# Performance work log

Hardware: AMD Instinct MI355X
Metric: run time of the kernel (lower is better)

The kernel has to match this reference:

```python
import jax, jax.numpy as jnp
import numpy as np

HEADS = 8
DIM_HEAD = 64
GAMMA = 0.01
LAMBDA_REG = 0.001
EPS = 1e-6


def layer_norm(x, g, b, eps=1e-5):
    mu = x.mean(-1, keepdims=True)
    var = jnp.var(x, axis=-1, keepdims=True)
    return (x - mu) * jax.lax.rsqrt(var + eps) * g + b


def setup_inputs() -> dict:
    key = jax.random.key(0)
    ks = jax.random.split(key, 20)
    B, N, DIM = 8, 1024, 512
    d = DIM_HEAD
    inner = HEADS * d
    inp = {}
    inp["q"] = jax.random.normal(ks[0], (B, N, DIM), jnp.float32)
    inp["k"] = jax.random.normal(ks[1], (B, N, DIM), jnp.float32)
    inp["v"] = jax.random.normal(ks[2], (B, N, DIM), jnp.float32)
    # input_linear: LayerNorm(dim) + Linear(dim -> inner, no bias)
    inp["ln_g"] = jnp.ones((DIM,), jnp.float32)
    inp["ln_b"] = jnp.zeros((DIM,), jnp.float32)
    inp["W_in"] = jax.random.normal(ks[3], (DIM, inner), jnp.float32) * 0.02
    # weight_predictor: Linear(2d->d), LN(d), ReLU, Linear(d->d//2), ReLU, Linear(d//2->3), Softmax
    inp["wp_W1"] = jax.random.normal(ks[4], (2 * d, d), jnp.float32) * 0.05
    inp["wp_b1"] = jnp.zeros((d,), jnp.float32)
    inp["wp_ln_g"] = jnp.ones((d,), jnp.float32)
    inp["wp_ln_b"] = jnp.zeros((d,), jnp.float32)
    inp["wp_W2"] = jax.random.normal(ks[5], (d, d // 2), jnp.float32) * 0.05
    inp["wp_b2"] = jnp.zeros((d // 2,), jnp.float32)
    inp["wp_W3"] = jax.random.normal(ks[6], (d // 2, 3), jnp.float32) * 0.05
    inp["wp_b3"] = jnp.zeros((3,), jnp.float32)
    inp["weight_temp"] = jnp.ones((1,), jnp.float32) * 2.0
    # output_linear: Linear(inner -> dim) with bias
    inp["W_out"] = jax.random.normal(ks[7], (inner, DIM), jnp.float32) * 0.02
    inp["b_out"] = jnp.zeros((DIM,), jnp.float32)
    return inp


def reference(q, k, v, ln_g, ln_b, W_in, wp_W1, wp_b1, wp_ln_g, wp_ln_b,
              wp_W2, wp_b2, wp_W3, wp_b3, weight_temp, W_out, b_out):
    H, d = HEADS, DIM_HEAD
    B, N, _ = q.shape

    def proj(t):
        x = layer_norm(t, ln_g, ln_b) @ W_in          # [B, N, H*d]
        return x.reshape(B, N, H, d).transpose(2, 0, 1, 3)  # h q n d

    f_q, f_k, f_v = proj(q), proj(k), proj(v)
    m = f_k.shape[2]

    # --- cosine component (cosine_distance with clamp to [-0.95, 0.95]) ---
    dots_raw = jnp.einsum('hbnd,hbmd->hbnm', f_q, f_k)
    n1 = jnp.linalg.norm(f_q, axis=-1, keepdims=True) + EPS      # h b n 1
    n2 = jnp.linalg.norm(f_k, axis=-1) + EPS                      # h b m
    cosine_sim = jnp.clip(dots_raw / (n1 * n2[:, :, None, :]), -0.95, 0.95)

    # --- regularized covariance component ---
    f_k_c = f_k - f_k.mean(axis=2, keepdims=True)
    f_q_c = f_q - f_q.mean(axis=-1, keepdims=True)
    cov = jnp.einsum('hbnd,hbmd->hbnm', f_q_c, f_k_c) / (d ** 0.5 + 1e-6)
    cov = jnp.clip((LAMBDA_REG / max(m, 1)) * cov, -20.0, 20.0)

    # --- margin-based variance component (eval: adaptive_gamma == gamma) ---
    fqn = f_q / jnp.maximum(jnp.linalg.norm(f_q, axis=-1, keepdims=True), EPS)
    fkn = f_k / jnp.maximum(jnp.linalg.norm(f_k, axis=-1, keepdims=True), EPS)
    cs = jnp.clip(jnp.einsum('hbnd,hbmd->hbnm', fqn, fkn), -0.95, 0.95)
    margin = jnp.clip(GAMMA - cs, 0.0, 5.0)
    var_full = jnp.broadcast_to(margin.mean(axis=-1, keepdims=True), cs.shape)

    # --- dynamic weight mixing ---
    q_g = f_q.mean(axis=(1, 2))   # [h, d]
    k_g = f_k.mean(axis=(1, 2))
    z = jnp.concatenate([q_g, k_g], axis=-1) @ wp_W1 + wp_b1
    z = jax.nn.relu(layer_norm(z, wp_ln_g, wp_ln_b))
    z = jax.nn.relu(z @ wp_W2 + wp_b2)
    p = jax.nn.softmax(z @ wp_W3 + wp_b3, axis=-1)   # predictor ends with Softmax
    wt = jnp.clip(weight_temp, 0.1, 10.0)
    w = jax.nn.softmax(p / wt, axis=-1)               # second softmax, as in torch
    w = w * (1.0 - 3 * 0.1) + 0.1                     # [h, 3]
    cw = w[:, 0][:, None, None, None]
    covw = w[:, 1][:, None, None, None]
    vw = w[:, 2][:, None, None, None]

    sg = jax.lax.stop_gradient
    std1 = lambda x: jnp.std(x, ddof=1)               # torch.std is unbiased
    cos_n = sg(std1(cosine_sim)) + EPS
    cov_n = sg(std1(cov)) + EPS
    var_n = sg(std1(var_full)) + EPS

    dots = cw * (cosine_sim / cos_n) + covw * (cov / cov_n * 0.3) + vw * (var_full / var_n * 0.3)
    temp = jnp.clip(0.5 + sg(std1(dots)), 0.3, 3.0)
    dots = dots / temp

    out = jnp.einsum('hbnm,hbmd->hbnd', jax.nn.softmax(dots, axis=-1), f_v)
    out = out.transpose(1, 2, 0, 3).reshape(B, N, H * d)
    return out @ W_out + b_out
```

## Files before the change

kernel.cpp:

```cpp
#include <hip/hip_runtime.h>
#include <math.h>

#define H_ 8
#define B_ 8
#define N_ 1024
#define D_ 64
#define DIMM 512
#define NROWS 8192

typedef __attribute__((ext_vector_type(8))) short s8v;
typedef __attribute__((ext_vector_type(4))) float f4v;
typedef __attribute__((ext_vector_type(2))) unsigned int u2v;
union fragu { s8v v; unsigned int w[4]; uint4 q; };

#define BMFMA(a, b, c) __builtin_amdgcn_mfma_f32_16x16x32_bf16(a, b, c, 0, 0, 0)

__device__ __forceinline__ float wred_sum(float v) {
#pragma unroll
    for (int m = 32; m >= 1; m >>= 1) v += __shfl_xor(v, m, 64);
    return v;
}
__device__ __forceinline__ double wred_sum_d(double v) {
#pragma unroll
    for (int m = 32; m >= 1; m >>= 1) v += __shfl_xor(v, m, 64);
    return v;
}
__device__ __forceinline__ unsigned cvtpk(float a, float b) {
    unsigned r;
    asm("v_cvt_pk_bf16_f32 %0, %1, %2" : "=v"(r) : "v"(a), "v"(b));
    return r;
}
__device__ __forceinline__ void bsplit(float a, unsigned short& hi, unsigned short& lo) {
    unsigned h = cvtpk(a, 0.f);
    hi = (unsigned short)h;
    float r = a - __uint_as_float(h << 16);
    lo = (unsigned short)cvtpk(r, 0.f);
}
__device__ __forceinline__ void split8(const float* a, unsigned* hw, unsigned* lw) {
#pragma unroll
    for (int i = 0; i < 4; ++i) {
        unsigned h = cvtpk(a[2 * i], a[2 * i + 1]);
        hw[i] = h;
        float l0 = a[2 * i]     - __uint_as_float(h << 16);
        float l1 = a[2 * i + 1] - __uint_as_float(h & 0xFFFF0000u);
        lw[i] = cvtpk(l0, l1);
    }
}

__device__ __forceinline__ float fexp2(float x) {
#if __has_builtin(__builtin_amdgcn_exp2f)
    return __builtin_amdgcn_exp2f(x);
#else
    return exp2f(x);
#endif
}

#if __has_builtin(__builtin_amdgcn_permlane16_swap) && __has_builtin(__builtin_amdgcn_permlane32_swap)
#define HAVE_PLSWAP 1
#endif

__device__ __forceinline__ float kbmax4(float x) {
#ifdef HAVE_PLSWAP
    u2v a = __builtin_amdgcn_permlane16_swap(__float_as_uint(x), __float_as_uint(x), false, false);
    float m = fmaxf(__uint_as_float(a[0]), __uint_as_float(a[1]));
    u2v c = __builtin_amdgcn_permlane32_swap(__float_as_uint(m), __float_as_uint(m), false, false);
    return fmaxf(__uint_as_float(c[0]), __uint_as_float(c[1]));
#else
    x = fmaxf(x, __shfl_xor(x, 16, 64));
    return fmaxf(x, __shfl_xor(x, 32, 64));
#endif
}
__device__ __forceinline__ float kbsum4(float x) {
#ifdef HAVE_PLSWAP
    u2v a = __builtin_amdgcn_permlane16_swap(__float_as_uint(x), __float_as_uint(x), false, false);
    float m = __uint_as_float(a[0]) + __uint_as_float(a[1]);
    u2v c = __builtin_amdgcn_permlane32_swap(__float_as_uint(m), __float_as_uint(m), false, false);
    return __uint_as_float(c[0]) + __uint_as_float(c[1]);
#else
    x += __shfl_xor(x, 16, 64);
    x += __shfl_xor(x, 32, 64);
    return x;
#endif
}

__global__ __launch_bounds__(256) void k_prep(
    const float* __restrict__ q, const float* __restrict__ k, const float* __restrict__ v,
    float* __restrict__ muv, float* __restrict__ rsd,
    const float* __restrict__ Win, const float* __restrict__ Wout,
    unsigned short* __restrict__ Wthi, unsigned short* __restrict__ Wtlo,
    unsigned short* __restrict__ Wothi, unsigned short* __restrict__ Wotlo)
{
    int bx = blockIdx.x;
    __shared__ float S[64][65];
    int t = threadIdx.x;
    if (bx < 6144) {
        int w = t >> 6, lane = t & 63;
        int row = bx * 4 + w;
        int tens = row >> 13;
        int lrow = row & 8191;
        const float* src = (tens == 0) ? q : (tens == 1 ? k : v);
        const float* p = src + (long long)lrow * DIMM + lane * 8;
        float4 a = *(const float4*)p;
        float4 b = *(const float4*)(p + 4);
        float s  = a.x + a.y + a.z + a.w + b.x + b.y + b.z + b.w;
        float sq = a.x*a.x + a.y*a.y + a.z*a.z + a.w*a.w + b.x*b.x + b.y*b.y + b.z*b.z + b.w*b.w;
        s = wred_sum(s); sq = wred_sum(sq);
        if (lane == 0) {
            float m = s * (1.f / 512.f);
            float var = sq * (1.f / 512.f) - m * m;
            muv[row] = m;
            rsd[row] = rsqrtf(var + 1e-5f);
        }
        return;
    }
    int sb = bx - 6144;
    int z = sb >> 6;
    int rem = sb & 63;
    int kxi = rem & 7, jxi = rem >> 3;
    const float* Wsrc = z ? Wout : Win;
    unsigned short* Dhi = z ? Wothi : Wthi;
    unsigned short* Dlo = z ? Wotlo : Wtlo;
    int k0 = kxi * 64, j0 = jxi * 64;
    int rr = t >> 2, seg = t & 3;
    const float* p = Wsrc + (long long)(k0 + rr) * DIMM + j0 + seg * 16;
    float4 a0 = *(const float4*)p, a1 = *(const float4*)(p + 4),
           a2 = *(const float4*)(p + 8), a3 = *(const float4*)(p + 12);
    S[rr][seg*16+ 0]=a0.x; S[rr][seg*16+ 1]=a0.y; S[rr][seg*16+ 2]=a0.z; S[rr][seg*16+ 3]=a0.w;
    S[rr][seg*16+ 4]=a1.x; S[rr][seg*16+ 5]=a1.y; S[rr][seg*16+ 6]=a1.z; S[rr][seg*16+ 7]=a1.w;
    S[rr][seg*16+ 8]=a2.x; S[rr][seg*16+ 9]=a2.y; S[rr][seg*16+10]=a2.z; S[rr][seg*16+11]=a2.w;
    S[rr][seg*16+12]=a3.x; S[rr][seg*16+13]=a3.y; S[rr][seg*16+14]=a3.z; S[rr][seg*16+15]=a3.w;
    __syncthreads();
    float f[16];
#pragma unroll
    for (int i = 0; i < 16; ++i) f[i] = S[seg * 16 + i][rr];
    unsigned hw[8], lw[8];
    split8(f, hw, lw);
    split8(f + 8, hw + 4, lw + 4);
    long long ob = (long long)(j0 + rr) * DIMM + k0 + seg * 16;
    *(uint4*)&Dhi[ob]     = make_uint4(hw[0], hw[1], hw[2], hw[3]);
    *(uint4*)&Dhi[ob + 8] = make_uint4(hw[4], hw[5], hw[6], hw[7]);
    *(uint4*)&Dlo[ob]     = make_uint4(lw[0], lw[1], lw[2], lw[3]);
    *(uint4*)&Dlo[ob + 8] = make_uint4(lw[4], lw[5], lw[6], lw[7]);
}

__global__ __launch_bounds__(256) void k_gemm_in(
    const float* __restrict__ qx, const float* __restrict__ kx, const float* __restrict__ vx,
    const float* __restrict__ muv, const float* __restrict__ rsd,
    const float* __restrict__ lng, const float* __restrict__ lnb,
    const unsigned short* __restrict__ Wthi, const unsigned short* __restrict__ Wtlo,
    unsigned short* __restrict__ Fqhi, unsigned short* __restrict__ Fqlo,
    unsigned short* __restrict__ Fkhi, unsigned short* __restrict__ Fklo,
    unsigned short* __restrict__ Fvthi, unsigned short* __restrict__ Fvtlo,
    float* __restrict__ qinv, float* __restrict__ mq,
    float* __restrict__ kinv, float* __restrict__ ks,
    float* __restrict__ csq, float* __restrict__ csk)
{
    int tens = blockIdx.z;
    const float* X = (tens == 0) ? qx : (tens == 1 ? kx : vx);
    int row0 = blockIdx.x * 128, hq = blockIdx.y;
    const float* muT = muv + tens * NROWS;
    const float* rsT = rsd + tens * NROWS;
    __shared__ unsigned short Ah[128][32], Al[128][32];
    __shared__ unsigned short Bh[128][32], Bl[128][32];
    int t = threadIdx.x;
    int w = t >> 6, lane = t & 63, l15 = lane & 15, kb = lane >> 4;
    int srow = t >> 1, sseg = t & 1;
    int sw = (srow >> 1) & 3;
    int c0 = ((2 * sseg + 0) ^ sw) * 8;
    int c1 = ((2 * sseg + 1) ^ sw) * 8;
    int rs = (l15 >> 1) & 3;
    int rb = (kb ^ rs) * 8;
    float amu = muT[row0 + srow], ars = rsT[row0 + srow];
    f4v acc[2][8];
#pragma unroll
    for (int rt = 0; rt < 2; ++rt)
#pragma unroll
        for (int dt = 0; dt < 8; ++dt) acc[rt][dt] = (f4v){0.f, 0.f, 0.f, 0.f};

    float4 x0, x1, x2, x3, g0, g1, g2, g3, cc0, cc1, cc2, cc3;
    uint4 wh0, wh1, wl0, wl1;
#define GIN_LOAD(KC) { \
    int kO = (KC) * 32 + sseg * 16; \
    const float* xp = X + (long long)(row0 + srow) * DIMM + kO; \
    x0 = *(const float4*)xp;       x1 = *(const float4*)(xp + 4); \
    x2 = *(const float4*)(xp + 8); x3 = *(const float4*)(xp + 12); \
    g0 = *(const float4*)(lng + kO);     g1 = *(const float4*)(lng + kO + 4); \
    g2 = *(const float4*)(lng + kO + 8); g3 = *(const float4*)(lng + kO + 12); \
    cc0 = *(const float4*)(lnb + kO);     cc1 = *(const float4*)(lnb + kO + 4); \
    cc2 = *(const float4*)(lnb + kO + 8); cc3 = *(const float4*)(lnb + kO + 12); \
    const unsigned short* wph = Wthi + (long long)(hq * 128 + srow) * DIMM + kO; \
    const unsigned short* wpl = Wtlo + (long long)(hq * 128 + srow) * DIMM + kO; \
    wh0 = *(const uint4*)wph; wh1 = *(const uint4*)(wph + 8); \
    wl0 = *(const uint4*)wpl; wl1 = *(const uint4*)(wpl + 8); }

    GIN_LOAD(0)
    for (int kc = 0; kc < 16; ++kc) {
        float av[16];
        av[ 0]=fmaf((x0.x-amu)*ars,g0.x,cc0.x); av[ 1]=fmaf((x0.y-amu)*ars,g0.y,cc0.y);
        av[ 2]=fmaf((x0.z-amu)*ars,g0.z,cc0.z); av[ 3]=fmaf((x0.w-amu)*ars,g0.w,cc0.w);
        av[ 4]=fmaf((x1.x-amu)*ars,g1.x,cc1.x); av[ 5]=fmaf((x1.y-amu)*ars,g1.y,cc1.y);
        av[ 6]=fmaf((x1.z-amu)*ars,g1.z,cc1.z); av[ 7]=fmaf((x1.w-amu)*ars,g1.w,cc1.w);
        av[ 8]=fmaf((x2.x-amu)*ars,g2.x,cc2.x); av[ 9]=fmaf((x2.y-amu)*ars,g2.y,cc2.y);
        av[10]=fmaf((x2.z-amu)*ars,g2.z,cc2.z); av[11]=fmaf((x2.w-amu)*ars,g2.w,cc2.w);
        av[12]=fmaf((x3.x-amu)*ars,g3.x,cc3.x); av[13]=fmaf((x3.y-amu)*ars,g3.y,cc3.y);
        av[14]=fmaf((x3.z-amu)*ars,g3.z,cc3.z); av[15]=fmaf((x3.w-amu)*ars,g3.w,cc3.w);
        unsigned hw[8], lw[8];
        split8(av, hw, lw);
        split8(av + 8, hw + 4, lw + 4);
        *(uint4*)&Ah[srow][c0] = make_uint4(hw[0], hw[1], hw[2], hw[3]);
        *(uint4*)&Ah[srow][c1] = make_uint4(hw[4], hw[5], hw[6], hw[7]);
        *(uint4*)&Al[srow][c0] = make_uint4(lw[0], lw[1], lw[2], lw[3]);
        *(uint4*)&Al[srow][c1] = make_uint4(lw[4], lw[5], lw[6], lw[7]);
        *(uint4*)&Bh[srow][c0] = wh0;
        *(uint4*)&Bh[srow][c1] = wh1;
        *(uint4*)&Bl[srow][c0] = wl0;
        *(uint4*)&Bl[srow][c1] = wl1;
        __syncthreads();
        if (kc < 15) { GIN_LOAD(kc + 1) }
        fragu ah[2], al2[2];
#pragma unroll
        for (int rt = 0; rt < 2; ++rt) {
            ah[rt].v  = *(const s8v*)&Ah[w * 32 + rt * 16 + l15][rb];
            al2[rt].v = *(const s8v*)&Al[w * 32 + rt * 16 + l15][rb];
        }
#pragma unroll
        for (int dt = 0; dt < 8; ++dt) {
            s8v bh = *(const s8v*)&Bh[dt * 16 + l15][rb];
            s8v bl = *(const s8v*)&Bl[dt * 16 + l15][rb];
#pragma unroll
            for (int rt = 0; rt < 2; ++rt) {
                acc[rt][dt] = BMFMA(ah[rt].v, bh, acc[rt][dt]);
                acc[rt][dt] = BMFMA(ah[rt].v, bl, acc[rt][dt]);
                acc[rt][dt] = BMFMA(al2[rt].v, bh, acc[rt][dt]);
            }
        }
        __syncthreads();
    }
#undef GIN_LOAD
    int b = row0 >> 10;
    if (tens < 2) {
        unsigned short* Dh = tens ? Fkhi : Fqhi;
        unsigned short* Dl = tens ? Fklo : Fqlo;
#pragma unroll
        for (int rt = 0; rt < 2; ++rt) {
            int nloc = (row0 & 1023) + w * 32 + rt * 16 + kb * 4;
#pragma unroll
            for (int dt = 0; dt < 8; ++dt) {
                int hb = (hq * 2 + (dt >> 2)) * 8 + b;
#pragma unroll
                for (int r = 0; r < 4; ++r) {
                    unsigned short hi, lo;
                    bsplit(acc[rt][dt][r], hi, lo);
                    long long idx = ((long long)hb * N_ + nloc + r) * D_ + (dt & 3) * 16 + l15;
                    Dh[idx] = hi;
                    Dl[idx] = lo;
                }
            }
#pragma unroll
            for (int hh = 0; hh < 2; ++hh) {
                int hb2 = (hq * 2 + hh) * 8 + b;
#pragma unroll
                for (int r = 0; r < 4; ++r) {
                    float a0 = acc[rt][hh*4+0][r], a1 = acc[rt][hh*4+1][r],
                          a2 = acc[rt][hh*4+2][r], a3 = acc[rt][hh*4+3][r];
                    float s  = a0 + a1 + a2 + a3;
                    float sq = a0*a0 + a1*a1 + a2*a2 + a3*a3;
#pragma unroll
                    for (int msk = 8; msk >= 1; msk >>= 1) {
                        s  += __shfl_xor(s, msk, 64);
                        sq += __shfl_xor(sq, msk, 64);
                    }
                    if (l15 == 0) {
                        int rowg = hb2 * N_ + nloc + r;
                        float inv = 1.f / (sqrtf(sq) + 1e-6f);
                        if (tens) { kinv[rowg] = inv; ks[rowg] = s; }
                        else      { qinv[rowg] = inv; mq[rowg] = s * (1.f / 64.f); }
                    }
                }
            }
        }
        float* cs = tens ? csk : csq;
#pragma unroll
        for (int dt = 0; dt < 8; ++dt) {
            int hb2 = (hq * 2 + (dt >> 2)) * 8 + b;
            float c = acc[0][dt][0] + acc[0][dt][1] + acc[0][dt][2] + acc[0][dt][3]
                    + acc[1][dt][0] + acc[1][dt][1] + acc[1][dt][2] + acc[1][dt][3];
            c += __shfl_xor(c, 16, 64);
            c += __shfl_xor(c, 32, 64);
            if (kb == 0) atomicAdd(&cs[hb2 * 64 + (dt & 3) * 16 + l15], c);
        }
    } else {
#pragma unroll
        for (int dt = 0; dt < 8; ++dt) {
            int hb = (hq * 2 + (dt >> 2)) * 8 + b;
#pragma unroll
            for (int rt = 0; rt < 2; ++rt) {
                int vcol = (row0 & 1023) + (w >> 1) * 64 + (w & 1) * 32 + (kb << 3) + (rt << 2);
                unsigned short hh4[4], ll4[4];
#pragma unroll
                for (int r = 0; r < 4; ++r) bsplit(acc[rt][dt][r], hh4[r], ll4[r]);
                long long idx = ((long long)hb * D_ + (dt & 3) * 16 + l15) * N_ + vcol;
                *(uint2*)&Fvthi[idx] = make_uint2((unsigned)hh4[0] | ((unsigned)hh4[1] << 16),
                                                  (unsigned)hh4[2] | ((unsigned)hh4[3] << 16));
                *(uint2*)&Fvtlo[idx] = make_uint2((unsigned)ll4[0] | ((unsigned)ll4[1] << 16),
                                                  (unsigned)ll4[2] | ((unsigned)ll4[3] << 16));
            }
        }
    }
}

__global__ __launch_bounds__(512) void k_gvec_mlp(
    const unsigned short* __restrict__ Fqhi, const unsigned short* __restrict__ Fqlo,
    const float* __restrict__ csk, const float* __restrict__ mq, float* __restrict__ g,
    const float* __restrict__ csq,
    const float* __restrict__ W1, const float* __restrict__ b1,
    const float* __restrict__ lg, const float* __restrict__ lb,
    const float* __restrict__ W2, const float* __restrict__ b2,
    const float* __restrict__ W3, const float* __restrict__ b3,
    const float* __restrict__ wtemp, float* __restrict__ wbuf)
{
    int bx = blockIdx.x;
    int t = threadIdx.x;
    if (bx < 128) {
        __shared__ float mk[64];
        __shared__ float smkv;
        int hb = bx >> 1;
        int r0 = (bx & 1) * 512;
        if (t < 64) mk[t] = csk[hb * 64 + t] * (1.f / 1024.f);
        __syncthreads();
        if (t == 0) {
            float s = 0;
            for (int i = 0; i < 64; ++i) s += mk[i];
            smkv = s;
        }
        __syncthreads();
        float smk = smkv;
        int rowg = hb * N_ + r0 + t;
        const uint4* ph = (const uint4*)(Fqhi + (long long)rowg * D_);
        const uint4* pl = (const uint4*)(Fqlo + (long long)rowg * D_);
        float acc = 0.f;
#pragma unroll
        for (int i = 0; i < 8; ++i) {
            uint4 hh = ph[i];
            uint4 ll = pl[i];
            const unsigned* hu = &hh.x;
            const unsigned* lu = &ll.x;
#pragma unroll
            for (int j = 0; j < 4; ++j) {
                float v0 = __uint_as_float((hu[j] & 0xFFFFu) << 16) + __uint_as_float((lu[j] & 0xFFFFu) << 16);
                float v1 = __uint_as_float(hu[j] & 0xFFFF0000u) + __uint_as_float(lu[j] & 0xFFFF0000u);
                acc = fmaf(v0, mk[i * 8 + j * 2], acc);
                acc = fmaf(v1, mk[i * 8 + j * 2 + 1], acc);
            }
        }
        g[rowg] = acc - mq[rowg] * smk;
        return;
    }
    __shared__ float cat[8][128];
    __shared__ float z1[8][64];
    __shared__ float zr[8][64];
    __shared__ float z2[8][32];
    __shared__ float z3[8][3];
    __shared__ float lnmu[8], lnrs[8];
    {
        int h = t >> 6, dd = t & 63;
        float sq = 0, sk = 0;
        for (int b = 0; b < 8; ++b) {
            sq += csq[(h * 8 + b) * 64 + dd];
            sk += csk[(h * 8 + b) * 64 + dd];
        }
        cat[h][dd]      = sq * (1.f / 8192.f);
        cat[h][64 + dd] = sk * (1.f / 8192.f);
    }
    __syncthreads();
    {
        int h = t >> 6, j = t & 63;
        float a = b1[j];
        for (int i = 0; i < 128; ++i) a = fmaf(cat[h][i], W1[i * 64 + j], a);
        z1[h][j] = a;
    }
    __syncthreads();
    if (t < 8) {
        float m = 0;
        for (int j = 0; j < 64; ++j) m += z1[t][j];
        m *= (1.f / 64.f);
        float v2 = 0;
        for (int j = 0; j < 64; ++j) { float d = z1[t][j] - m; v2 += d * d; }
        v2 *= (1.f / 64.f);
        lnmu[t] = m; lnrs[t] = rsqrtf(v2 + 1e-5f);
    }
    __syncthreads();
    {
        int h = t >> 6, j = t & 63;
        float z = (z1[h][j] - lnmu[h]) * lnrs[h] * lg[j] + lb[j];
        zr[h][j] = fmaxf(z, 0.f);
    }
    __syncthreads();
    if (t < 256) {
        int h = t >> 5, j2 = t & 31;
        float a = b2[j2];
        for (int j = 0; j < 64; ++j) a = fmaf(zr[h][j], W2[j * 32 + j2], a);
        z2[h][j2] = fmaxf(a, 0.f);
    }
    __syncthreads();
    if (t < 24) {
        int h = t / 3, c = t % 3;
        float a = b3[c];
        for (int j2 = 0; j2 < 32; ++j2) a = fmaf(z2[h][j2], W3[j2 * 3 + c], a);
        z3[h][c] = a;
    }
    __syncthreads();
    if (t < 8) {
        int h = t;
        float wt = fminf(fmaxf(wtemp[0], 0.1f), 10.f);
        float a = z3[h][0], b = z3[h][1], c = z3[h][2];
        float mx = fmaxf(a, fmaxf(b, c));
        float ea = expf(a - mx), eb = expf(b - mx), ec = expf(c - mx);
        float s = ea + eb + ec;
        float p0 = ea / s, p1 = eb / s, p2 = ec / s;
        float q0 = p0 / wt, q1 = p1 / wt, q2 = p2 / wt;
        mx = fmaxf(q0, fmaxf(q1, q2));
        ea = expf(q0 - mx); eb = expf(q1 - mx); ec = expf(q2 - mx);
        s = ea + eb + ec;
        wbuf[h * 3 + 0] = (ea / s) * 0.7f + 0.1f;
        wbuf[h * 3 + 1] = (eb / s) * 0.7f + 0.1f;
        wbuf[h * 3 + 2] = (ec / s) * 0.7f + 0.1f;
    }
}

__global__ __launch_bounds__(256) void k_pass1(
    const unsigned short* __restrict__ Fqhi, const unsigned short* __restrict__ Fkhi,
    const float* __restrict__ qinvA, const float* __restrict__ mqA, const float* __restrict__ gA,
    const float* __restrict__ kinvA, const float* __restrict__ ksA,
    float* __restrict__ rowA, float* __restrict__ rowM,
    double* __restrict__ accum)
{
    int bx = blockIdx.x;
    int loc = bx >> 3;
    int hb = (bx & 7) * 8 + (loc >> 6);
    int rem = loc & 63;
    int n0 = (rem >> 2) * 64;
    int mtc = rem & 3;
    int h = hb >> 3;
    __shared__ unsigned short Khi[64][72];
    __shared__ float ki1s[64], ksls[64];
    __shared__ double wsum[4][4];
    int t = threadIdx.x;
    int w = t >> 6, lane = t & 63, l15 = lane & 15, kb = lane >> 4;
    int srow = t >> 2, seg = t & 3;
    const float SC = (float)((0.001 / 1024.0) / (8.0 + 1e-6));

    fragu qh[2];
    {
        long long qbase = ((long long)hb * N_ + n0 + w * 16 + l15) * D_;
#pragma unroll
        for (int k2 = 0; k2 < 2; ++k2)
            qh[k2].q = *(const uint4*)(Fqhi + qbase + k2 * 32 + kb * 8);
    }
    float qi1_r[4], qm_r[4], qgs_r[4];
#pragma unroll
    for (int r = 0; r < 4; ++r) {
        int rowg = hb * N_ + n0 + w * 16 + kb * 4 + r;
        qi1_r[r] = qinvA[rowg];
        qm_r[r]  = mqA[rowg];
        qgs_r[r] = gA[rowg] * SC;
    }
    float sacc[5][4] = {};

    for (int mt = mtc * 4; mt < mtc * 4 + 4; ++mt) {
        {
            long long kro = ((long long)hb * N_ + mt * 64 + srow) * D_ + seg * 16;
            uint4 h0 = *(const uint4*)(Fkhi + kro), h1 = *(const uint4*)(Fkhi + kro + 8);
            *(uint4*)&Khi[srow][seg * 16]     = h0;
            *(uint4*)&Khi[srow][seg * 16 + 8] = h1;
            if (t < 64) {
                ki1s[t] = kinvA[hb * N_ + mt * 64 + t];
                ksls[t] = ksA[hb * N_ + mt * 64 + t];
            }
        }
        __syncthreads();
#pragma unroll
        for (int nt = 0; nt < 4; ++nt) {
            f4v acc = {0.f, 0.f, 0.f, 0.f};
            s8v kh0 = *(const s8v*)&Khi[nt * 16 + l15][kb * 8];
            s8v kh1 = *(const s8v*)&Khi[nt * 16 + l15][32 + kb * 8];
            acc = BMFMA(qh[0].v, kh0, acc);
            acc = BMFMA(qh[1].v, kh1, acc);
            int key = nt * 16 + l15;
            float k1 = ki1s[key];
            float ksvSC = ksls[key] * SC;
            float e_r[4];
#pragma unroll
            for (int r = 0; r < 4; ++r) e_r[r] = fmaf(qm_r[r], ksvSC, qgs_r[r]);
#pragma unroll
            for (int r = 0; r < 4; ++r) {
                float dv = acc[r];
                float A  = dv * qi1_r[r] * k1;
                float Bv = fmaf(dv, SC, -e_r[r]);
                sacc[0][r] += A;
                sacc[1][r] = fmaf(A, A, sacc[1][r]);
                sacc[2][r] = fmaf(Bv, Bv, sacc[2][r]);
                sacc[3][r] = fmaf(A, Bv, sacc[3][r]);
                sacc[4][r] += fminf(A, 0.01f);
            }
        }
        __syncthreads();
    }
    {
        const int map[4] = {0, 3, 4, 6};
#pragma unroll
        for (int qq = 0; qq < 4; ++qq) {
            float s = sacc[qq][0] + sacc[qq][1] + sacc[qq][2] + sacc[qq][3];
            double d = wred_sum_d((double)s);
            if (lane == 0) wsum[qq][w] = d;
        }
        __syncthreads();
        if (t < 4) {
            double tot = wsum[t][0] + wsum[t][1] + wsum[t][2] + wsum[t][3];
            atomicAdd(&accum[h * 9 + map[t]], tot);
        }
    }
    float vA[4], vM[4];
#pragma unroll
    for (int r = 0; r < 4; ++r) {
        float a = sacc[0][r], m = sacc[4][r];
#pragma unroll
        for (int msk = 8; msk >= 1; msk >>= 1) {
            a += __shfl_xor(a, msk, 64);
            m += __shfl_xor(m, msk, 64);
        }
        vA[r] = a; vM[r] = m;
    }
    if (l15 == 0) {
#pragma unroll
        for (int r = 0; r < 4; ++r) {
            int rowg = hb * N_ + n0 + w * 16 + kb * 4 + r;
            atomicAdd(&rowA[rowg], vA[r]);
            atomicAdd(&rowM[rowg], 2.56f - vM[r]);
        }
    }
}

__global__ __launch_bounds__(256) void k_rowfin(
    const float* __restrict__ rowA, const float* __restrict__ rowM,
    float* __restrict__ varC, double* __restrict__ accum,
    const float* __restrict__ wbuf, float* __restrict__ scl,
    unsigned* __restrict__ ticket)
{
    int hb = blockIdx.x;
    int h = hb >> 3;
    int t = threadIdx.x;
    int w = t >> 6, lane = t & 63;
    __shared__ double wsum[3][4];
    double c2 = 0, c5 = 0, c7 = 0;
    for (int i = t; i < N_; i += 256) {
        int idx = hb * N_ + i;
        float rm = rowM[idx];
        float C = rm * (1.f / 1024.f);
        varC[idx] = C;
        c2 += (double)rm;
        c5 += (double)rm * (double)C;
        c7 += (double)C * (double)rowA[idx];
    }
    c2 = wred_sum_d(c2); c5 = wred_sum_d(c5); c7 = wred_sum_d(c7);
    if (lane == 0) { wsum[0][w] = c2; wsum[1][w] = c5; wsum[2][w] = c7; }
    __syncthreads();
    if (t < 3) {
        const int map[3] = {2, 5, 7};
        double tot = wsum[t][0] + wsum[t][1] + wsum[t][2] + wsum[t][3];
        atomicAdd(&accum[h * 9 + map[t]], tot);
    }
    __syncthreads();
    __shared__ unsigned lastv;
    if (t == 0) {
        __threadfence();
        lastv = atomicAdd(ticket, 1u);
    }
    __syncthreads();
    if (lastv != 63 || t != 0) return;

    double av[8][9];
#pragma unroll
    for (int hh = 0; hh < 8; ++hh)
#pragma unroll
        for (int j = 0; j < 9; ++j)
            av[hh][j] = __hip_atomic_load(&accum[hh * 9 + j], __ATOMIC_RELAXED, __HIP_MEMORY_SCOPE_AGENT);
    const double T = 67108864.0;
    double GA = 0, GB = 0, GC = 0, GAA = 0, GBB = 0, GCC = 0;
#pragma unroll
    for (int hh = 0; hh < 8; ++hh) {
        GA += av[hh][0]; GB += av[hh][1]; GC += av[hh][2];
        GAA += av[hh][3]; GBB += av[hh][4]; GCC += av[hh][5];
    }
    double cos_n = sqrt(fmax((GAA - GA * GA / T) / (T - 1.0), 0.0)) + 1e-6;
    double cov_n = sqrt(fmax((GBB - GB * GB / T) / (T - 1.0), 0.0)) + 1e-6;
    double var_n = sqrt(fmax((GCC - GC * GC / T) / (T - 1.0), 0.0)) + 1e-6;
    double sd = 0, sd2 = 0;
    double al[8], be[8], ga[8];
#pragma unroll
    for (int hh = 0; hh < 8; ++hh) {
        al[hh] = (double)wbuf[hh * 3 + 0] / cos_n;
        be[hh] = (double)wbuf[hh * 3 + 1] * 0.3 / cov_n;
        ga[hh] = (double)wbuf[hh * 3 + 2] * 0.3 / var_n;
        sd  += al[hh] * av[hh][0] + be[hh] * av[hh][1] + ga[hh] * av[hh][2];
        sd2 += al[hh] * al[hh] * av[hh][3] + be[hh] * be[hh] * av[hh][4] + ga[hh] * ga[hh] * av[hh][5]
             + 2.0 * al[hh] * be[hh] * av[hh][6] + 2.0 * al[hh] * ga[hh] * av[hh][7]
             + 2.0 * be[hh] * ga[hh] * av[hh][8];
    }
    double vard = fmax((sd2 - sd * sd / T) / (T - 1.0), 0.0);
    double temp = 0.5 + sqrt(vard);
    temp = fmin(fmax(temp, 0.3), 3.0);
#pragma unroll
    for (int hh = 0; hh < 8; ++hh) {
        scl[hh * 3 + 0] = (float)(al[hh] / temp);
        scl[hh * 3 + 1] = (float)(be[hh] / temp);
        scl[hh * 3 + 2] = (float)(ga[hh] / temp);
    }
}

__global__ __launch_bounds__(512) void k_pass2(
    const unsigned short* __restrict__ Fqhi, const unsigned short* __restrict__ Fqlo,
    const unsigned short* __restrict__ Fkhi, const unsigned short* __restrict__ Fklo,
    const unsigned short* __restrict__ Fvthi, const unsigned short* __restrict__ Fvtlo,
    const float* __restrict__ qinvA, const float* __restrict__ mqA, const float* __restrict__ gA,
    const float* __restrict__ kinvA, const float* __restrict__ ksA,
    const float* __restrict__ varC, const float* __restrict__ scl,
    unsigned short* __restrict__ attn_hi, unsigned short* __restrict__ attn_lo)
{
    int bx = blockIdx.x;
    int g = bx >> 3;
    int hb = (bx & 7) * 8 + (g >> 3);
    int n0 = (g & 7) * 128;
    int h = hb >> 3, b = hb & 7;
    __shared__ unsigned short Khi[2][64][72];
    __shared__ unsigned short Klo[2][64][72];
    __shared__ unsigned short Vh[2][64][72];
    __shared__ unsigned short Vl[2][64][72];
    __shared__ float ki1s[2][64], ksls[2][64];
    int t = threadIdx.x;
    int w = t >> 6, lane = t & 63, l15 = lane & 15, kb = lane >> 4;
    int srow = t >> 3, sc = (t & 7) * 8;
    const float SC = (float)((0.001 / 1024.0) / (8.0 + 1e-6));
    const float L2E = 1.44269504f;
    float sAh = scl[h*3+0] * L2E, sBh = scl[h*3+1] * L2E, sCh = scl[h*3+2] * L2E;

    fragu qh[2], ql[2];
    {
        long long qbase = ((long long)hb * N_ + n0 + w * 16 + l15) * D_;
#pragma unroll
        for (int k2 = 0; k2 < 2; ++k2) {
            qh[k2].q = *(const uint4*)(Fqhi + qbase + k2 * 32 + kb * 8);
            ql[k2].q = *(const uint4*)(Fqlo + qbase + k2 * 32 + kb * 8);
        }
    }
    int rowq = hb * N_ + n0 + w * 16 + l15;
    float qiA  = qinvA[rowq] * sAh;
    float SCb  = SC * sBh;
    float nqmS = -mqA[rowq] * SCb;
    float cb  = fmaf(sCh, varC[rowq], -(gA[rowq] * SC) * sBh);

    float Mr = -1e30f, Lr = 0.f;
    f4v oacc[4];
#pragma unroll
    for (int dt = 0; dt < 4; ++dt) oacc[dt] = (f4v){0.f, 0.f, 0.f, 0.f};
    int idxr[4];
#pragma unroll
    for (int r = 0; r < 4; ++r) idxr[r] = (kb * 20 + r) * 4;

    uint4 rkh, rkl, rvh, rvl;
    float rki, rks;
#define P2_LOAD(MT) { \
    long long kro = ((long long)hb * N_ + (MT) * 64 + srow) * D_ + sc; \
    rkh = *(const uint4*)(Fkhi + kro); rkl = *(const uint4*)(Fklo + kro); \
    long long vro = ((long long)hb * D_ + srow) * N_ + (MT) * 64 + sc; \
    rvh = *(const uint4*)(Fvthi + vro); rvl = *(const uint4*)(Fvtlo + vro); \
    if (t < 64) { rki = kinvA[hb * N_ + (MT) * 64 + t]; rks = ksA[hb * N_ + (MT) * 64 + t]; } }

    P2_LOAD(0)
    for (int mt = 0; mt < 16; ++mt) {
        int buf = mt & 1;
        *(uint4*)&Khi[buf][srow][sc] = rkh;
        *(uint4*)&Klo[buf][srow][sc] = rkl;
        *(uint4*)&Vh[buf][srow][sc]  = rvh;
        *(uint4*)&Vl[buf][srow][sc]  = rvl;
        if (t < 64) { ki1s[buf][t] = rki; ksls[buf][t] = rks; }
        __syncthreads();
        if (mt < 15) { P2_LOAD(mt + 1) }
        float p[4][4];
#pragma unroll
        for (int nt = 0; nt < 4; ++nt) {
            f4v acc = {0.f, 0.f, 0.f, 0.f};
            __builtin_amdgcn_s_setprio(1);
#pragma unroll
            for (int k2 = 0; k2 < 2; ++k2) {
                s8v kh = *(const s8v*)&Khi[buf][nt * 16 + l15][k2 * 32 + kb * 8];
                s8v kl = *(const s8v*)&Klo[buf][nt * 16 + l15][k2 * 32 + kb * 8];
                acc = BMFMA(kh, qh[k2].v, acc);
                acc = BMFMA(kh, ql[k2].v, acc);
                acc = BMFMA(kl, qh[k2].v, acc);
            }
            __builtin_amdgcn_s_setprio(0);
            float4 k1v = *(const float4*)&ki1s[buf][nt * 16 + kb * 4];
            float4 ksv = *(const float4*)&ksls[buf][nt * 16 + kb * 4];
            float k1a[4] = {k1v.x, k1v.y, k1v.z, k1v.w};
            float ksa[4] = {ksv.x, ksv.y, ksv.z, ksv.w};
#pragma unroll
            for (int r = 0; r < 4; ++r) {
                float qks = fmaf(qiA, k1a[r], SCb);
                float cbk = fmaf(nqmS, ksa[r], cb);
                p[nt][r] = fmaf(acc[r], qks, cbk);
            }
        }
        float tmax = fmaxf(fmaxf(fmaxf(p[0][0], p[0][1]), fmaxf(p[0][2], p[0][3])),
                           fmaxf(fmaxf(p[1][0], p[1][1]), fmaxf(p[1][2], p[1][3])));
        tmax = fmaxf(tmax, fmaxf(fmaxf(fmaxf(p[2][0], p[2][1]), fmaxf(p[2][2], p[2][3])),
                                 fmaxf(fmaxf(p[3][0], p[3][1]), fmaxf(p[3][2], p[3][3]))));
        tmax = kbmax4(tmax);
        if (__any(tmax - Mr > 11.5415605f)) {
            float nM = fmaxf(Mr, tmax);
            float scf = fexp2(Mr - nM);
            Mr = nM;
            Lr *= scf;
            float scr[4];
#pragma unroll
            for (int r = 0; r < 4; ++r)
                scr[r] = __int_as_float(__builtin_amdgcn_ds_bpermute(idxr[r], __float_as_int(scf)));
#pragma unroll
            for (int dt = 0; dt < 4; ++dt)
#pragma unroll
                for (int r = 0; r < 4; ++r) oacc[dt][r] *= scr[r];
        }
        float ps = 0.f;
#pragma unroll
        for (int nt = 0; nt < 4; ++nt)
#pragma unroll
            for (int r = 0; r < 4; ++r) {
                float e = fexp2(p[nt][r] - Mr);
                p[nt][r] = e;
                ps += e;
            }
        ps = kbsum4(ps);
        Lr += ps;
        fragu pah[2], pal[2];
#pragma unroll
        for (int k2 = 0; k2 < 2; ++k2) {
#pragma unroll
            for (int j = 0; j < 4; ++j) {
                float x = p[2 * k2 + (j >> 1)][(j & 1) * 2];
                float y = p[2 * k2 + (j >> 1)][(j & 1) * 2 + 1];
                unsigned hw2 = cvtpk(x, y);
                pah[k2].w[j] = hw2;
                float lx = x - __uint_as_float(hw2 << 16);
                float ly = y - __uint_as_float(hw2 & 0xFFFF0000u);
                pal[k2].w[j] = cvtpk(lx, ly);
            }
        }
        __builtin_amdgcn_s_setprio(1);
#pragma unroll
        for (int dt = 0; dt < 4; ++dt) {
#pragma unroll
            for (int k2 = 0; k2 < 2; ++k2) {
                s8v vh2 = *(const s8v*)&Vh[buf][dt * 16 + l15][k2 * 32 + kb * 8];
                s8v vl2 = *(const s8v*)&Vl[buf][dt * 16 + l15][k2 * 32 + kb * 8];
                oacc[dt] = BMFMA(pah[k2].v, vh2, oacc[dt]);
                oacc[dt] = BMFMA(pah[k2].v, vl2, oacc[dt]);
                oacc[dt] = BMFMA(pal[k2].v, vh2, oacc[dt]);
            }
        }
        __builtin_amdgcn_s_setprio(0);
    }
#undef P2_LOAD
    float inv_r[4];
#pragma unroll
    for (int r = 0; r < 4; ++r) {
        float Lq = __int_as_float(__builtin_amdgcn_ds_bpermute(idxr[r], __float_as_int(Lr)));
        inv_r[r] = 1.f / Lq;
    }
#pragma unroll
    for (int dt = 0; dt < 4; ++dt)
#pragma unroll
        for (int r = 0; r < 4; ++r) {
            float o = oacc[dt][r] * inv_r[r];
            unsigned short hi, lo;
            bsplit(o, hi, lo);
            long long idx = ((long long)(b * N_ + n0 + w * 16 + kb * 4 + r)) * DIMM + h * 64 + dt * 16 + l15;
            attn_hi[idx] = hi;
            attn_lo[idx] = lo;
        }
}

__global__ __launch_bounds__(256) void k_gemm_out(
    const unsigned short* __restrict__ Ahi, const unsigned short* __restrict__ Alo,
    const unsigned short* __restrict__ Wothi, const unsigned short* __restrict__ Wotlo,
    const float* __restrict__ bias, float* __restrict__ out)
{
    int row0 = blockIdx.x * 128, j0 = blockIdx.y * 128;
    __shared__ unsigned short Ah[128][32], Al[128][32];
    __shared__ unsigned short Bh[128][32], Bl[128][32];
    int t = threadIdx.x;
    int w = t >> 6, lane = t & 63, l15 = lane & 15, kb = lane >> 4;
    int srow = t >> 1, sseg = t & 1;
    int sw = (srow >> 1) & 3;
    int c0 = ((2 * sseg + 0) ^ sw) * 8;
    int c1 = ((2 * sseg + 1) ^ sw) * 8;
    int rs = (l15 >> 1) & 3;
    int rb = (kb ^ rs) * 8;
    f4v acc[2][8];
#pragma unroll
    for (int rt = 0; rt < 2; ++rt)
#pragma unroll
        for (int dt = 0; dt < 8; ++dt) acc[rt][dt] = (f4v){0.f, 0.f, 0.f, 0.f};
    uint4 a0, a1, al0, al1, b0, b1, bl0, bl1;
#define GOUT_LOAD(KC) { \
    int kO = (KC) * 32 + sseg * 16; \
    const unsigned short* ap  = Ahi + (long long)(row0 + srow) * DIMM + kO; \
    const unsigned short* alp = Alo + (long long)(row0 + srow) * DIMM + kO; \
    a0 = *(const uint4*)ap;  a1 = *(const uint4*)(ap + 8); \
    al0 = *(const uint4*)alp; al1 = *(const uint4*)(alp + 8); \
    const unsigned short* bp  = Wothi + (long long)(j0 + srow) * DIMM + kO; \
    const unsigned short* blp = Wotlo + (long long)(j0 + srow) * DIMM + kO; \
    b0 = *(const uint4*)bp;  b1 = *(const uint4*)(bp + 8); \
    bl0 = *(const uint4*)blp; bl1 = *(const uint4*)(blp + 8); }

    GOUT_LOAD(0)
    for (int kc = 0; kc < 16; ++kc) {
        *(uint4*)&Ah[srow][c0] = a0;
        *(uint4*)&Ah[srow][c1] = a1;
        *(uint4*)&Al[srow][c0] = al0;
        *(uint4*)&Al[srow][c1] = al1;
        *(uint4*)&Bh[srow][c0] = b0;
        *(uint4*)&Bh[srow][c1] = b1;
        *(uint4*)&Bl[srow][c0] = bl0;
        *(uint4*)&Bl[srow][c1] = bl1;
        __syncthreads();
        if (kc < 15) { GOUT_LOAD(kc + 1) }
        fragu ah[2], al2[2];
#pragma unroll
        for (int rt = 0; rt < 2; ++rt) {
            ah[rt].v  = *(const s8v*)&Ah[w * 32 + rt * 16 + l15][rb];
            al2[rt].v = *(const s8v*)&Al[w * 32 + rt * 16 + l15][rb];
        }
#pragma unroll
        for (int dt = 0; dt < 8; ++dt) {
            s8v bh = *(const s8v*)&Bh[dt * 16 + l15][rb];
            s8v bl = *(const s8v*)&Bl[dt * 16 + l15][rb];
#pragma unroll
            for (int rt = 0; rt < 2; ++rt) {
                acc[rt][dt] = BMFMA(ah[rt].v, bh, acc[rt][dt]);
                acc[rt][dt] = BMFMA(ah[rt].v, bl, acc[rt][dt]);
                acc[rt][dt] = BMFMA(al2[rt].v, bh, acc[rt][dt]);
            }
        }
        __syncthreads();
    }
#undef GOUT_LOAD
#pragma unroll
    for (int dt = 0; dt < 8; ++dt) {
        float bv = bias[j0 + dt * 16 + l15];
#pragma unroll
        for (int rt = 0; rt < 2; ++rt)
#pragma unroll
            for (int r = 0; r < 4; ++r)
                out[(long long)(row0 + w * 32 + rt * 16 + kb * 4 + r) * DIMM + j0 + dt * 16 + l15]
                    = acc[rt][dt][r] + bv;
    }
}

extern "C" void kernel_launch(void* const* d_in, const int* in_sizes, int n_in,
                              void* d_out, int out_size, void* d_ws, size_t ws_size,
                              hipStream_t stream) {
    (void)in_sizes; (void)n_in; (void)out_size; (void)ws_size;
    const float* q      = (const float*)d_in[0];
    const float* k      = (const float*)d_in[1];
    const float* v      = (const float*)d_in[2];
    const float* ln_g   = (const float*)d_in[3];
    const float* ln_b   = (const float*)d_in[4];
    const float* W_in   = (const float*)d_in[5];
    const float* wp_W1  = (const float*)d_in[6];
    const float* wp_b1  = (const float*)d_in[7];
    const float* wp_lng = (const float*)d_in[8];
    const float* wp_lnb = (const float*)d_in[9];
    const float* wp_W2  = (const float*)d_in[10];
    const float* wp_b2  = (const float*)d_in[11];
    const float* wp_W3  = (const float*)d_in[12];
    const float* wp_b3  = (const float*)d_in[13];
    const float* wtemp  = (const float*)d_in[14];
    const float* W_out  = (const float*)d_in[15];
    const float* b_out  = (const float*)d_in[16];
    float* out = (float*)d_out;

    char* w = (char*)d_ws;
    unsigned short* attn_hi = (unsigned short*)(w + 0);
    unsigned short* attn_lo = (unsigned short*)(w + 8388608);
    unsigned short* Fqhi  = (unsigned short*)(w + 16777216);
    unsigned short* Fqlo  = (unsigned short*)(w + 25165824);
    unsigned short* Fkhi  = (unsigned short*)(w + 33554432);
    unsigned short* Fklo  = (unsigned short*)(w + 41943040);
    unsigned short* Fvthi = (unsigned short*)(w + 50331648);
    unsigned short* Fvtlo = (unsigned short*)(w + 58720256);
    unsigned short* Wthi  = (unsigned short*)(w + 67108864);
    unsigned short* Wtlo  = (unsigned short*)(w + 67633152);
    unsigned short* Wothi = (unsigned short*)(w + 68157440);
    unsigned short* Wotlo = (unsigned short*)(w + 68681728);
    float* muv  = (float*)(w + 69206016);
    float* rsd  = (float*)(w + 69304320);
    float* qinv = (float*)(w + 69402624);
    float* mq   = (float*)(w + 69664768);
    float* gv   = (float*)(w + 69926912);
    float* kinv = (float*)(w + 70189056);
    float* ks   = (float*)(w + 70451200);
    float* vc   = (float*)(w + 70713344);
    float* rowA = (float*)(w + 70975488);
    float* rowB = (float*)(w + 71237632);
    float* rowM = (float*)(w + 71499776);
    float* csq  = (float*)(w + 71761920);
    float* csk  = (float*)(w + 71778304);
    double* acc = (double*)(w + 71794688);
    float* wb   = (float*)(w + 71796736);
    float* scl  = (float*)(w + 71796864);
    unsigned* ticket = (unsigned*)(w + 71794688 + 768);
    (void)rowB;

    hipMemsetAsync(rowA, 0, 3 * 262144 + 2 * 16384 + 2048, stream);

    k_prep<<<6272, 256, 0, stream>>>(q, k, v, muv, rsd, W_in, W_out, Wthi, Wtlo, Wothi, Wotlo);
    k_gemm_in<<<dim3(64, 4, 3), 256, 0, stream>>>(q, k, v, muv, rsd, ln_g, ln_b,
                                                  Wthi, Wtlo, Fqhi, Fqlo, Fkhi, Fklo, Fvthi, Fvtlo,
                                                  qinv, mq, kinv, ks, csq, csk);
    k_gvec_mlp<<<129, 512, 0, stream>>>(Fqhi, Fqlo, csk, mq, gv, csq,
                                        wp_W1, wp_b1, wp_lng, wp_lnb, wp_W2, wp_b2, wp_W3, wp_b3,
                                        wtemp, wb);
    k_pass1<<<4096, 256, 0, stream>>>(Fqhi, Fkhi, qinv, mq, gv, kinv, ks, rowA, rowM, acc);
    k_rowfin<<<64, 256, 0, stream>>>(rowA, rowM, vc, acc, wb, scl, ticket);
    k_pass2<<<512, 512, 0, stream>>>(Fqhi, Fqlo, Fkhi, Fklo, Fvthi, Fvtlo,
                                     qinv, mq, gv, kinv, ks, vc, scl, attn_hi, attn_lo);
    k_gemm_out<<<dim3(64, 4), 256, 0, stream>>>(attn_hi, attn_lo, Wothi, Wotlo, b_out, out);
}
```

Measured before the change: 220.3 us.

## Process two query tiles per wave in attention pass to reuse K/V tiles

Each wave in the flash-attention pass now handles 32 query rows as two 16-row tiles with separate softmax states, so each block covers 256 query rows and the grid is halved to 256 blocks. Every K/V tile staged in shared memory, and every fragment read from it, now feeds twice as many MFMAs, which halves global K/V traffic and LDS reads per unit of work. The cost is roughly doubled accumulator and fragment registers per thread, made explicit with a launch-bounds occupancy hint. The smaller grid may also leave compute units underused on a 256-CU part.

```diff
diff --git a/kernel.cpp b/kernel.cpp
--- a/kernel.cpp
+++ b/kernel.cpp
@@ -618,7 +618,7 @@
     }
 }
 
-__global__ __launch_bounds__(512) void k_pass2(
+__global__ __launch_bounds__(512, 2) void k_pass2(
     const unsigned short* __restrict__ Fqhi, const unsigned short* __restrict__ Fqlo,
     const unsigned short* __restrict__ Fkhi, const unsigned short* __restrict__ Fklo,
     const unsigned short* __restrict__ Fvthi, const unsigned short* __restrict__ Fvtlo,
@@ -629,8 +629,8 @@
 {
     int bx = blockIdx.x;
     int g = bx >> 3;
-    int hb = (bx & 7) * 8 + (g >> 3);
-    int n0 = (g & 7) * 128;
+    int hb = (bx & 7) * 8 + (g >> 2);
+    int n0 = (g & 3) * 256;
     int h = hb >> 3, b = hb & 7;
     __shared__ unsigned short Khi[2][64][72];
     __shared__ unsigned short Klo[2][64][72];
@@ -643,26 +643,36 @@
     const float SC = (float)((0.001 / 1024.0) / (8.0 + 1e-6));
     const float L2E = 1.44269504f;
     float sAh = scl[h*3+0] * L2E, sBh = scl[h*3+1] * L2E, sCh = scl[h*3+2] * L2E;
-
-    fragu qh[2], ql[2];
+    float SCb = SC * sBh;
+
+    fragu qh0[2], ql0[2], qh1[2], ql1[2];
+    int rowq0 = hb * N_ + n0 + w * 32 + l15;
+    int rowq1 = rowq0 + 16;
     {
-        long long qbase = ((long long)hb * N_ + n0 + w * 16 + l15) * D_;
+        long long qb0 = (long long)rowq0 * D_;
+        long long qb1 = (long long)rowq1 * D_;
 #pragma unroll
         for (int k2 = 0; k2 < 2; ++k2) {
-            qh[k2].q = *(const uint4*)(Fqhi + qbase + k2 * 32 + kb * 8);
-            ql[k2].q = *(const uint4*)(Fqlo + qbase + k2 * 32 + kb * 8);
-        }
-    }
-    int rowq = hb * N_ + n0 + w * 16 + l15;
-    float qiA  = qinvA[rowq] * sAh;
-    float SCb  = SC * sBh;
-    float nqmS = -mqA[rowq] * SCb;
-    float cb  = fmaf(sCh, varC[rowq], -(gA[rowq] * SC) * sBh);
-
-    float Mr = -1e30f, Lr = 0.f;
-    f4v oacc[4];
-#pragma unroll
-    for (int dt = 0; dt < 4; ++dt) oacc[dt] = (f4v){0.f, 0.f, 0.f, 0.f};
+            qh0[k2].q = *(const uint4*)(Fqhi + qb0 + k2 * 32 + kb * 8);
+            ql0[k2].q = *(const uint4*)(Fqlo + qb0 + k2 * 32 + kb * 8);
+            qh1[k2].q = *(const uint4*)(Fqhi + qb1 + k2 * 32 + kb * 8);
+            ql1[k2].q = *(const uint4*)(Fqlo + qb1 + k2 * 32 + kb * 8);
+        }
+    }
+    float qiA0 = qinvA[rowq0] * sAh;
+    float qiA1 = qinvA[rowq1] * sAh;
+    float nqmS0 = -mqA[rowq0] * SCb;
+    float nqmS1 = -mqA[rowq1] * SCb;
+    float cb0 = fmaf(sCh, varC[rowq0], -(gA[rowq0] * SC) * sBh);
+    float cb1 = fmaf(sCh, varC[rowq1], -(gA[rowq1] * SC) * sBh);
+
+    float Mr0 = -1e30f, Lr0 = 0.f, Mr1 = -1e30f, Lr1 = 0.f;
+    f4v oacc0[4], oacc1[4];
+#pragma unroll
+    for (int dt = 0; dt < 4; ++dt) {
+        oacc0[dt] = (f4v){0.f, 0.f, 0.f, 0.f};
+        oacc1[dt] = (f4v){0.f, 0.f, 0.f, 0.f};
+    }
     int idxr[4];
 #pragma unroll
     for (int r = 0; r < 4; ++r) idxr[r] = (kb * 20 + r) * 4;
@@ -686,18 +696,22 @@
         if (t < 64) { ki1s[buf][t] = rki; ksls[buf][t] = rks; }
         __syncthreads();
         if (mt < 15) { P2_LOAD(mt + 1) }
-        float p[4][4];
+        float p0[4][4], p1[4][4];
 #pragma unroll
         for (int nt = 0; nt < 4; ++nt) {
-            f4v acc = {0.f, 0.f, 0.f, 0.f};
+            f4v a0 = {0.f, 0.f, 0.f, 0.f};
+            f4v a1 = {0.f, 0.f, 0.f, 0.f};
             __builtin_amdgcn_s_setprio(1);
 #pragma unroll
             for (int k2 = 0; k2 < 2; ++k2) {
                 s8v kh = *(const s8v*)&Khi[buf][nt * 16 + l15][k2 * 32 + kb * 8];
                 s8v kl = *(const s8v*)&Klo[buf][nt * 16 + l15][k2 * 32 + kb * 8];
-                acc = BMFMA(kh, qh[k2].v, acc);
-                acc = BMFMA(kh, ql[k2].v, acc);
-                acc = BMFMA(kl, qh[k2].v, acc);
+                a0 = BMFMA(kh, qh0[k2].v, a0);
+                a0 = BMFMA(kh, ql0[k2].v, a0);
+                a0 = BMFMA(kl, qh0[k2].v, a0);
+                a1 = BMFMA(kh, qh1[k2].v, a1);
+                a1 = BMFMA(kh, ql1[k2].v, a1);
+                a1 = BMFMA(kl, qh1[k2].v, a1);
             }
             __builtin_amdgcn_s_setprio(0);
             float4 k1v = *(const float4*)&ki1s[buf][nt * 16 + kb * 4];
@@ -706,53 +720,101 @@
             float ksa[4] = {ksv.x, ksv.y, ksv.z, ksv.w};
 #pragma unroll
             for (int r = 0; r < 4; ++r) {
-                float qks = fmaf(qiA, k1a[r], SCb);
-                float cbk = fmaf(nqmS, ksa[r], cb);
-                p[nt][r] = fmaf(acc[r], qks, cbk);
-            }
-        }
-        float tmax = fmaxf(fmaxf(fmaxf(p[0][0], p[0][1]), fmaxf(p[0][2], p[0][3])),
-                           fmaxf(fmaxf(p[1][0], p[1][1]), fmaxf(p[1][2], p[1][3])));
-        tmax = fmaxf(tmax, fmaxf(fmaxf(fmaxf(p[2][0], p[2][1]), fmaxf(p[2][2], p[2][3])),
-                                 fmaxf(fmaxf(p[3][0], p[3][1]), fmaxf(p[3][2], p[3][3]))));
-        tmax = kbmax4(tmax);
-        if (__any(tmax - Mr > 11.5415605f)) {
-            float nM = fmaxf(Mr, tmax);
-            float scf = fexp2(Mr - nM);
-            Mr = nM;
-            Lr *= scf;
-            float scr[4];
-#pragma unroll
-            for (int r = 0; r < 4; ++r)
-                scr[r] = __int_as_float(__builtin_amdgcn_ds_bpermute(idxr[r], __float_as_int(scf)));
-#pragma unroll
-            for (int dt = 0; dt < 4; ++dt)
-#pragma unroll
-                for (int r = 0; r < 4; ++r) oacc[dt][r] *= scr[r];
-        }
-        float ps = 0.f;
-#pragma unroll
-        for (int nt = 0; nt < 4; ++nt)
-#pragma unroll
-            for (int r = 0; r < 4; ++r) {
-                float e = fexp2(p[nt][r] - Mr);
-                p[nt][r] = e;
-                ps += e;
-            }
-        ps = kbsum4(ps);
-        Lr += ps;
-        fragu pah[2], pal[2];
-#pragma unroll
-        for (int k2 = 0; k2 < 2; ++k2) {
-#pragma unroll
-            for (int j = 0; j < 4; ++j) {
-                float x = p[2 * k2 + (j >> 1)][(j & 1) * 2];
-                float y = p[2 * k2 + (j >> 1)][(j & 1) * 2 + 1];
-                unsigned hw2 = cvtpk(x, y);
-                pah[k2].w[j] = hw2;
-                float lx = x - __uint_as_float(hw2 << 16);
-                float ly = y - __uint_as_float(hw2 & 0xFFFF0000u);
-                pal[k2].w[j] = cvtpk(lx, ly);
+                p0[nt][r] = fmaf(a0[r], fmaf(qiA0, k1a[r], SCb), fmaf(nqmS0, ksa[r], cb0));
+                p1[nt][r] = fmaf(a1[r], fmaf(qiA1, k1a[r], SCb), fmaf(nqmS1, ksa[r], cb1));
+            }
+        }
+        fragu pah0[2], pal0[2], pah1[2], pal1[2];
+        {
+            float tmax = fmaxf(fmaxf(fmaxf(p0[0][0], p0[0][1]), fmaxf(p0[0][2], p0[0][3])),
+                               fmaxf(fmaxf(p0[1][0], p0[1][1]), fmaxf(p0[1][2], p0[1][3])));
+            tmax = fmaxf(tmax, fmaxf(fmaxf(fmaxf(p0[2][0], p0[2][1]), fmaxf(p0[2][2], p0[2][3])),
+                                     fmaxf(fmaxf(p0[3][0], p0[3][1]), fmaxf(p0[3][2], p0[3][3]))));
+            tmax = kbmax4(tmax);
+            if (__any(tmax - Mr0 > 11.5415605f)) {
+                float nM = fmaxf(Mr0, tmax);
+                float scf = fexp2(Mr0 - nM);
+                Mr0 = nM;
+                Lr0 *= scf;
+                float s0 = __int_as_float(__builtin_amdgcn_ds_bpermute(idxr[0], __float_as_int(scf)));
+                float s1 = __int_as_float(__builtin_amdgcn_ds_bpermute(idxr[1], __float_as_int(scf)));
+                float s2 = __int_as_float(__builtin_amdgcn_ds_bpermute(idxr[2], __float_as_int(scf)));
+                float s3 = __int_as_float(__builtin_amdgcn_ds_bpermute(idxr[3], __float_as_int(scf)));
+#pragma unroll
+                for (int dt = 0; dt < 4; ++dt) {
+                    oacc0[dt][0] *= s0; oacc0[dt][1] *= s1;
+                    oacc0[dt][2] *= s2; oacc0[dt][3] *= s3;
+                }
+            }
+            float ps = 0.f;
+#pragma unroll
+            for (int nt = 0; nt < 4; ++nt)
+#pragma unroll
+                for (int r = 0; r < 4; ++r) {
+                    float e = fexp2(p0[nt][r] - Mr0);
+                    p0[nt][r] = e;
+                    ps += e;
+                }
+            ps = kbsum4(ps);
+            Lr0 += ps;
+#pragma unroll
+            for (int k2 = 0; k2 < 2; ++k2) {
+#pragma unroll
+                for (int j = 0; j < 4; ++j) {
+                    float x = p0[2 * k2 + (j >> 1)][(j & 1) * 2];
+                    float y = p0[2 * k2 + (j >> 1)][(j & 1) * 2 + 1];
+                    unsigned hw2 = cvtpk(x, y);
+                    pah0[k2].w[j] = hw2;
+                    float lx = x - __uint_as_float(hw2 << 16);
+                    float ly = y - __uint_as_float(hw2 & 0xFFFF0000u);
+                    pal0[k2].w[j] = cvtpk(lx, ly);
+                }
+            }
+        }
+        {
+            float tmax = fmaxf(fmaxf(fmaxf(p1[0][0], p1[0][1]), fmaxf(p1[0][2], p1[0][3])),
+                               fmaxf(fmaxf(p1[1][0], p1[1][1]), fmaxf(p1[1][2], p1[1][3])));
+            tmax = fmaxf(tmax, fmaxf(fmaxf(fmaxf(p1[2][0], p1[2][1]), fmaxf(p1[2][2], p1[2][3])),
+                                     fmaxf(fmaxf(p1[3][0], p1[3][1]), fmaxf(p1[3][2], p1[3][3]))));
+            tmax = kbmax4(tmax);
+            if (__any(tmax - Mr1 > 11.5415605f)) {
+                float nM = fmaxf(Mr1, tmax);
+                float scf = fexp2(Mr1 - nM);
+                Mr1 = nM;
+                Lr1 *= scf;
+                float s0 = __int_as_float(__builtin_amdgcn_ds_bpermute(idxr[0], __float_as_int(scf)));
+                float s1 = __int_as_float(__builtin_amdgcn_ds_bpermute(idxr[1], __float_as_int(scf)));
+                float s2 = __int_as_float(__builtin_amdgcn_ds_bpermute(idxr[2], __float_as_int(scf)));
+                float s3 = __int_as_float(__builtin_amdgcn_ds_bpermute(idxr[3], __float_as_int(scf)));
+#pragma unroll
+                for (int dt = 0; dt < 4; ++dt) {
+                    oacc1[dt][0] *= s0; oacc1[dt][1] *= s1;
+                    oacc1[dt][2] *= s2; oacc1[dt][3] *= s3;
+                }
+            }
+            float ps = 0.f;
+#pragma unroll
+            for (int nt = 0; nt < 4; ++nt)
+#pragma unroll
+                for (int r = 0; r < 4; ++r) {
+                    float e = fexp2(p1[nt][r] - Mr1);
+                    p1[nt][r] = e;
+                    ps += e;
+                }
+            ps = kbsum4(ps);
+            Lr1 += ps;
+#pragma unroll
+            for (int k2 = 0; k2 < 2; ++k2) {
+#pragma unroll
+                for (int j = 0; j < 4; ++j) {
+                    float x = p1[2 * k2 + (j >> 1)][(j & 1) * 2];
+                    float y = p1[2 * k2 + (j >> 1)][(j & 1) * 2 + 1];
+                    unsigned hw2 = cvtpk(x, y);
+                    pah1[k2].w[j] = hw2;
+                    float lx = x - __uint_as_float(hw2 << 16);
+                    float ly = y - __uint_as_float(hw2 & 0xFFFF0000u);
+                    pal1[k2].w[j] = cvtpk(lx, ly);
+                }
             }
         }
         __builtin_amdgcn_s_setprio(1);
@@ -762,31 +824,55 @@
             for (int k2 = 0; k2 < 2; ++k2) {
                 s8v vh2 = *(const s8v*)&Vh[buf][dt * 16 + l15][k2 * 32 + kb * 8];
                 s8v vl2 = *(const s8v*)&Vl[buf][dt * 16 + l15][k2 * 32 + kb * 8];
-                oacc[dt] = BMFMA(pah[k2].v, vh2, oacc[dt]);
-                oacc[dt] = BMFMA(pah[k2].v, vl2, oacc[dt]);
-                oacc[dt] = BMFMA(pal[k2].v, vh2, oacc[dt]);
+                oacc0[dt] = BMFMA(pah0[k2].v, vh2, oacc0[dt]);
+                oacc0[dt] = BMFMA(pah0[k2].v, vl2, oacc0[dt]);
+                oacc0[dt] = BMFMA(pal0[k2].v, vh2, oacc0[dt]);
+                oacc1[dt] = BMFMA(pah1[k2].v, vh2, oacc1[dt]);
+                oacc1[dt] = BMFMA(pah1[k2].v, vl2, oacc1[dt]);
+                oacc1[dt] = BMFMA(pal1[k2].v, vh2, oacc1[dt]);
             }
         }
         __builtin_amdgcn_s_setprio(0);
     }
 #undef P2_LOAD
-    float inv_r[4];
-#pragma unroll
-    for (int r = 0; r < 4; ++r) {
-        float Lq = __int_as_float(__builtin_amdgcn_ds_bpermute(idxr[r], __float_as_int(Lr)));
-        inv_r[r] = 1.f / Lq;
-    }
-#pragma unroll
-    for (int dt = 0; dt < 4; ++dt)
-#pragma unroll
-        for (int r = 0; r < 4; ++r) {
-            float o = oacc[dt][r] * inv_r[r];
-            unsigned short hi, lo;
-            bsplit(o, hi, lo);
-            long long idx = ((long long)(b * N_ + n0 + w * 16 + kb * 4 + r)) * DIMM + h * 64 + dt * 16 + l15;
-            attn_hi[idx] = hi;
-            attn_lo[idx] = lo;
-        }
+    {
+        float i0 = 1.f / __int_as_float(__builtin_amdgcn_ds_bpermute(idxr[0], __float_as_int(Lr0)));
+        float i1 = 1.f / __int_as_float(__builtin_amdgcn_ds_bpermute(idxr[1], __float_as_int(Lr0)));
+        float i2 = 1.f / __int_as_float(__builtin_amdgcn_ds_bpermute(idxr[2], __float_as_int(Lr0)));
+        float i3 = 1.f / __int_as_float(__builtin_amdgcn_ds_bpermute(idxr[3], __float_as_int(Lr0)));
+        float inv_r[4] = {i0, i1, i2, i3};
+#pragma unroll
+        for (int dt = 0; dt < 4; ++dt)
+#pragma unroll
+            for (int r = 0; r < 4; ++r) {
+                float o = oacc0[dt][r] * inv_r[r];
+                unsigned short hi, lo;
+                bsplit(o, hi, lo);
+                long long idx = ((long long)(b * N_ + n0 + w * 32 + kb * 4 + r)) * DIMM
+                              + h * 64 + dt * 16 + l15;
+                attn_hi[idx] = hi;
+                attn_lo[idx] = lo;
+            }
+    }
+    {
+        float i0 = 1.f / __int_as_float(__builtin_amdgcn_ds_bpermute(idxr[0], __float_as_int(Lr1)));
+        float i1 = 1.f / __int_as_float(__builtin_amdgcn_ds_bpermute(idxr[1], __float_as_int(Lr1)));
+        float i2 = 1.f / __int_as_float(__builtin_amdgcn_ds_bpermute(idxr[2], __float_as_int(Lr1)));
+        float i3 = 1.f / __int_as_float(__builtin_amdgcn_ds_bpermute(idxr[3], __float_as_int(Lr1)));
+        float inv_r[4] = {i0, i1, i2, i3};
+#pragma unroll
+        for (int dt = 0; dt < 4; ++dt)
+#pragma unroll
+            for (int r = 0; r < 4; ++r) {
+                float o = oacc1[dt][r] * inv_r[r];
+                unsigned short hi, lo;
+                bsplit(o, hi, lo);
+                long long idx = ((long long)(b * N_ + n0 + w * 32 + 16 + kb * 4 + r)) * DIMM
+                              + h * 64 + dt * 16 + l15;
+                attn_hi[idx] = hi;
+                attn_lo[idx] = lo;
+            }
+    }
 }
 
 __global__ __launch_bounds__(256) void k_gemm_out(
@@ -932,7 +1018,7 @@
                                         wtemp, wb);
     k_pass1<<<4096, 256, 0, stream>>>(Fqhi, Fkhi, qinv, mq, gv, kinv, ks, rowA, rowM, acc);
     k_rowfin<<<64, 256, 0, stream>>>(rowA, rowM, vc, acc, wb, scl, ticket);
-    k_pass2<<<512, 512, 0, stream>>>(Fqhi, Fqlo, Fkhi, Fklo, Fvthi, Fvtlo,
+    k_pass2<<<256, 512, 0, stream>>>(Fqhi, Fqlo, Fkhi, Fklo, Fvthi, Fvtlo,
                                      qinv, mq, gv, kinv, ks, vc, scl, attn_hi, attn_lo);
     k_gemm_out<<<dim3(64, 4), 256, 0, stream>>>(attn_hi, attn_lo, Wothi, Wotlo, b_out, out);
 }
```

Result: no change. 216.8 us (-1.6%).
